# Optimization experiments

Measured on AMD Instinct MI355X. Metric: run time of the kernel, lower is better.

The kernel has to match this reference:

```python
import jax, jax.numpy as jnp
import numpy as np

N = 100000
E = 1600000
IN_CH = 128
HEADS = 4
OUT_CH = 32


def setup_inputs() -> dict:
    key = jax.random.key(0)
    k1, k2, k3, k4, k5, k6 = jax.random.split(key, 6)
    x = jax.random.normal(k1, (N, IN_CH), dtype=jnp.float32)
    edge_attr = jax.random.normal(k2, (E,), dtype=jnp.float32)
    edge_index = jax.random.randint(k3, (2, E), 0, N, dtype=jnp.int64)
    # xavier-uniform-ish parameter init
    def xavier(k, shape):
        fan_in, fan_out = shape[-1], shape[-2] if len(shape) > 1 else shape[-1]
        lim = jnp.sqrt(6.0 / (fan_in + fan_out)).astype(jnp.float32)
        return jax.random.uniform(k, shape, jnp.float32, -lim, lim)
    lin_w = xavier(k4, (HEADS * OUT_CH, IN_CH))       # nn.Linear weight [out,in]
    lin_edge_w = xavier(k5, (HEADS * OUT_CH, 1))      # [out,1]
    att = xavier(k6, (1, HEADS, 3 * OUT_CH))
    return {"x": x, "edge_attr": edge_attr, "edge_index": edge_index,
            "lin_w": lin_w, "lin_edge_w": lin_edge_w, "att": att}


def reference(x, edge_attr, edge_index, lin_w, lin_edge_w, att):
    n = x.shape[0]
    # node transform: [N, H, C]
    xh = (x @ lin_w.T).reshape(n, HEADS, OUT_CH)
    # edge transform: [E, H, C]
    eh = (edge_attr[:, None] @ lin_edge_w.T).reshape(-1, HEADS, OUT_CH)
    row, col = edge_index[0], edge_index[1]
    # split att into source/dest/edge parts to avoid materializing cat([x_i,x_j,e])
    att_i, att_j, att_e = jnp.split(att, 3, axis=-1)  # each [1, H, C]
    # per-edge attention logits: [E, H]
    alpha = ((xh[row] * att_i).sum(-1)
             + (xh[col] * att_j).sum(-1)
             + (eh * att_e).sum(-1))
    alpha = jax.nn.leaky_relu(alpha, negative_slope=0.2)
    # segment softmax over destination node (row)
    amax = jax.ops.segment_max(alpha, row, num_segments=n)           # [N, H]
    amax = jnp.where(jnp.isfinite(amax), amax, 0.0)
    ex = jnp.exp(alpha - amax[row])
    den = jax.ops.segment_sum(ex, row, num_segments=n)               # [N, H]
    alpha = ex / (den[row] + 1e-16)
    # weighted message scatter-add: [N, H, C]
    out = jax.ops.segment_sum(alpha[..., None] * xh[col], row, num_segments=n)
    # concat heads
    return out.reshape(n, HEADS * OUT_CH)
```

## Files before the change

### kernel.cpp

```cpp
#include <hip/hip_runtime.h>

#define HEADS 4
#define OUT_CH 32
#define HC 128
#define INC 128
#define CAP 48

typedef __attribute__((ext_vector_type(8))) short bfrag;
typedef __attribute__((ext_vector_type(4))) float ffrag;

union U16 { uint4 u; bfrag f; };

__device__ __forceinline__ unsigned short f2bf(float f) {
  unsigned int u = __float_as_uint(f);
  unsigned int r = (u + 0x7FFFu + ((u >> 16) & 1u)) >> 16;
  return (unsigned short)r;
}

__global__ __launch_bounds__(256) void prep_kernel(
    const float* __restrict__ W, const float* __restrict__ lew,
    const float* __restrict__ att, unsigned short* __restrict__ Wb,
    float* __restrict__ ce, int* __restrict__ cnt, int N) {
  int bid = blockIdx.x;
  int tid = threadIdx.x;
  if (bid < 16) {
    int i4 = bid * 256 + tid;
    float4 v = ((const float4*)W)[i4];
    ushort4 o;
    o.x = f2bf(v.x);
    o.y = f2bf(v.y);
    o.z = f2bf(v.z);
    o.w = f2bf(v.w);
    ((ushort4*)Wb)[i4] = o;
    if (bid == 0 && tid < HEADS) {
      float s = 0.f;
      for (int c = 0; c < OUT_CH; ++c)
        s += lew[tid * OUT_CH + c] * att[tid * 96 + 2 * OUT_CH + c];
      ce[tid] = s;
    }
  } else {
    int zi = (bid - 16) * 256 + tid;
    int stride = (gridDim.x - 16) * 256;
    for (int i = zi; i < N; i += stride) cnt[i] = 0;
  }
}

#define APITCH 136
__global__ __launch_bounds__(256) void gemm_build(
    const float* __restrict__ x, const unsigned short* __restrict__ Wb,
    const float* __restrict__ att, const int* __restrict__ ei,
    const float* __restrict__ ea, unsigned short* __restrict__ xhb,
    float* __restrict__ si, float* __restrict__ sj, int* __restrict__ cnt,
    unsigned int* __restrict__ slots, int nrows, int E, int G) {
  __shared__ unsigned short Als[4][16 * APITCH];

  if (blockIdx.x >= G) {
    int e = (blockIdx.x - G) * 256 + threadIdx.x;
    if (e < E) {
      int r = ei[e];
      int c = ei[E + e];
      unsigned int u = __float_as_uint(ea[e]);
      unsigned int word = ((u + 0x10000u) & 0xFFFE0000u) | (unsigned int)c;
      int pos = atomicAdd(&cnt[r], 1);
      if (pos < CAP) slots[(size_t)r * CAP + pos] = word;
    }
    return;
  }

  const int tid = threadIdx.x;
  const int wid = tid >> 6;
  const int lane = tid & 63;
  const int row0 = blockIdx.x * 64 + wid * 16;
  if (row0 >= nrows) return;
  unsigned short* As = &Als[wid][0];

#pragma unroll
  for (int t = 0; t < 8; t++) {
    int idx = t * 64 + lane;
    int r = idx >> 5;
    int q = idx & 31;
    int gr = row0 + r;
    float4 v = make_float4(0.f, 0.f, 0.f, 0.f);
    if (gr < nrows) v = ((const float4*)x)[(size_t)gr * 32 + q];
    unsigned int p0 = ((unsigned int)f2bf(v.y) << 16) | f2bf(v.x);
    unsigned int p1 = ((unsigned int)f2bf(v.w) << 16) | f2bf(v.z);
    *(uint2*)&As[r * APITCH + q * 4] = make_uint2(p0, p1);
  }

  const int m15 = lane & 15;
  const int g = lane >> 4;

  ffrag acc[8];
#pragma unroll
  for (int t = 0; t < 8; t++) acc[t] = (ffrag){0.f, 0.f, 0.f, 0.f};

#pragma unroll
  for (int ks = 0; ks < 4; ks++) {
    U16 a;
    a.u = *(const uint4*)&As[m15 * APITCH + ks * 32 + g * 8];
#pragma unroll
    for (int nt = 0; nt < 8; nt++) {
      U16 b;
      b.u = *(const uint4*)&Wb[(size_t)(nt * 16 + m15) * 128 + ks * 32 + g * 8];
      acc[nt] = __builtin_amdgcn_mfma_f32_16x16x32_bf16(a.f, b.f, acc[nt],
                                                        0, 0, 0);
    }
  }

  float ai[8], aj[8];
#pragma unroll
  for (int t = 0; t < 8; t++) {
    int h = t >> 1, c = (t & 1) * 16 + m15;
    ai[t] = att[h * 96 + c];
    aj[t] = att[h * 96 + 32 + c];
  }
#pragma unroll
  for (int reg = 0; reg < 4; reg++) {
    float ph_i[4], ph_j[4];
#pragma unroll
    for (int h = 0; h < 4; h++) {
      ph_i[h] = acc[2 * h][reg] * ai[2 * h] + acc[2 * h + 1][reg] * ai[2 * h + 1];
      ph_j[h] = acc[2 * h][reg] * aj[2 * h] + acc[2 * h + 1][reg] * aj[2 * h + 1];
    }
#pragma unroll
    for (int off = 8; off >= 1; off >>= 1) {
#pragma unroll
      for (int h = 0; h < 4; h++) {
        ph_i[h] += __shfl_down(ph_i[h], off, 16);
        ph_j[h] += __shfl_down(ph_j[h], off, 16);
      }
    }
    int gr = row0 + g * 4 + reg;
    if (m15 == 0 && gr < nrows) {
#pragma unroll
      for (int h = 0; h < 4; h++) {
        si[(size_t)gr * 4 + h] = ph_i[h];
        sj[(size_t)gr * 4 + h] = ph_j[h];
      }
    }
  }

#pragma unroll
  for (int t = 0; t < 8; t++) {
#pragma unroll
    for (int reg = 0; reg < 4; reg++) {
      int r = g * 4 + reg;
      int n = t * 16 + m15;
      As[r * 128 + n] = f2bf(acc[t][reg]);
    }
  }
  const uint4* src = (const uint4*)As;
#pragma unroll
  for (int t = 0; t < 4; t++) {
    int idx = t * 64 + lane;
    int r = idx >> 4, q = idx & 15;
    int gr = row0 + r;
    if (gr < nrows) ((uint4*)(xhb + (size_t)gr * 128))[q] = src[idx];
  }
}

__global__ __launch_bounds__(256) void gather_kernel(
    const int* __restrict__ cnt, const unsigned int* __restrict__ slots,
    const float* __restrict__ si, const float* __restrict__ sj,
    const float* __restrict__ ce, const unsigned short* __restrict__ xhb,
    float* __restrict__ out, int n) {
  __shared__ int cls[4][CAP];
  __shared__ float wls[4][4][CAP];

  int wid = threadIdx.x >> 6;
  int node = blockIdx.x * 4 + wid;
  if (node >= n) return;
  int lane = threadIdx.x & 63;
  int h = lane >> 4;

  int m = cnt[node];
  float4 si4 = *(const float4*)(si + (size_t)node * 4);
  float4 ce4 = *(const float4*)ce;

  if (lane < CAP) {
    unsigned int word = slots[(size_t)node * CAP + lane];
    int c = word & 0x1FFFF;
    if (c >= n) c = 0;
    float eaf = __uint_as_float(word & 0xFFFE0000u);
    float4 sjv = *(const float4*)(sj + (size_t)c * 4);
    float t0 = si4.x + sjv.x + eaf * ce4.x;
    float t1 = si4.y + sjv.y + eaf * ce4.y;
    float t2 = si4.z + sjv.z + eaf * ce4.z;
    float t3 = si4.w + sjv.w + eaf * ce4.w;
    t0 = t0 > 0.f ? t0 : 0.2f * t0;
    t1 = t1 > 0.f ? t1 : 0.2f * t1;
    t2 = t2 > 0.f ? t2 : 0.2f * t2;
    t3 = t3 > 0.f ? t3 : 0.2f * t3;
    bool live = lane < m;
    cls[wid][lane] = live ? c : 0;
    wls[wid][0][lane] = live ? __expf(t0) : 0.f;
    wls[wid][1][lane] = live ? __expf(t1) : 0.f;
    wls[wid][2][lane] = live ? __expf(t2) : 0.f;
    wls[wid][3][lane] = live ? __expf(t3) : 0.f;
  }
  if (m > CAP) m = CAP;
  int mr = (m + 7) & ~7;

  const unsigned short* xb = xhb + lane * 2;
  float acc0 = 0.f, acc1 = 0.f, wsum = 0.f;
  for (int k = 0; k < mr; k += 8) {
    int4 ca = *(const int4*)&cls[wid][k];
    int4 cb = *(const int4*)&cls[wid][k + 4];
    float4 wa = *(const float4*)&wls[wid][h][k];
    float4 wb = *(const float4*)&wls[wid][h][k + 4];
    unsigned int x0 = *(const unsigned int*)(xb + (size_t)ca.x * 128);
    unsigned int x1 = *(const unsigned int*)(xb + (size_t)ca.y * 128);
    unsigned int x2 = *(const unsigned int*)(xb + (size_t)ca.z * 128);
    unsigned int x3 = *(const unsigned int*)(xb + (size_t)ca.w * 128);
    unsigned int x4 = *(const unsigned int*)(xb + (size_t)cb.x * 128);
    unsigned int x5 = *(const unsigned int*)(xb + (size_t)cb.y * 128);
    unsigned int x6 = *(const unsigned int*)(xb + (size_t)cb.z * 128);
    unsigned int x7 = *(const unsigned int*)(xb + (size_t)cb.w * 128);
    acc0 += wa.x * __uint_as_float(x0 << 16) +
            wa.y * __uint_as_float(x1 << 16) +
            wa.z * __uint_as_float(x2 << 16) +
            wa.w * __uint_as_float(x3 << 16) +
            wb.x * __uint_as_float(x4 << 16) +
            wb.y * __uint_as_float(x5 << 16) +
            wb.z * __uint_as_float(x6 << 16) +
            wb.w * __uint_as_float(x7 << 16);
    acc1 += wa.x * __uint_as_float(x0 & 0xFFFF0000u) +
            wa.y * __uint_as_float(x1 & 0xFFFF0000u) +
            wa.z * __uint_as_float(x2 & 0xFFFF0000u) +
            wa.w * __uint_as_float(x3 & 0xFFFF0000u) +
            wb.x * __uint_as_float(x4 & 0xFFFF0000u) +
            wb.y * __uint_as_float(x5 & 0xFFFF0000u) +
            wb.z * __uint_as_float(x6 & 0xFFFF0000u) +
            wb.w * __uint_as_float(x7 & 0xFFFF0000u);
    wsum += wa.x + wa.y + wa.z + wa.w + wb.x + wb.y + wb.z + wb.w;
  }

  float inv = 1.0f / (wsum + 1e-16f);
  float2 o;
  o.x = acc0 * inv;
  o.y = acc1 * inv;
  *(float2*)(out + (size_t)node * HC + lane * 2) = o;
}

extern "C" void kernel_launch(void* const* d_in, const int* in_sizes, int n_in,
                              void* d_out, int out_size, void* d_ws,
                              size_t ws_size, hipStream_t stream) {
  const float* x = (const float*)d_in[0];
  const float* edge_attr = (const float*)d_in[1];
  const int* ei = (const int*)d_in[2];
  const float* lin_w = (const float*)d_in[3];
  const float* lew = (const float*)d_in[4];
  const float* att = (const float*)d_in[5];
  float* out = (float*)d_out;

  const int N = in_sizes[0] / INC;
  const int E = in_sizes[1];

  unsigned int* slots = (unsigned int*)d_ws;
  unsigned short* xhb = (unsigned short*)(slots + (size_t)N * CAP);
  float* si = (float*)(xhb + (size_t)N * 128);
  float* sj = si + (size_t)N * 4;
  float* ce = sj + (size_t)N * 4;
  unsigned short* Wb = (unsigned short*)(ce + 16);
  int* cnt = (int*)(Wb + 16384);

  prep_kernel<<<128, 256, 0, stream>>>(lin_w, lew, att, Wb, ce, cnt, N);

  const int G = (N + 63) / 64;
  const int B = (E + 255) / 256;
  gemm_build<<<G + B, 256, 0, stream>>>(x, Wb, att, ei, edge_attr, xhb, si,
                                        sj, cnt, slots, N, E, G);
  gather_kernel<<<(N + 3) / 4, 256, 0, stream>>>(cnt, slots, si, sj, ce, xhb,
                                                 out, N);
}
```

Baseline: 278.8 us.

## Bucket edges by destination range before atomic slot scatter for locality

Edge binning no longer does random atomics directly. Each wave first partitions its edges into 8 destination-node ranges with ballots and writes them to per-wave queues, reusing the output buffer as scratch. A new scatter kernel then processes one range per block group, so the atomics and slot writes touch a smaller working set that fits better in cache. This adds an extra kernel launch plus queue write/read traffic, and edges past the per-wave capacity fall back to the direct atomic path.

```diff
diff --git a/kernel.cpp b/kernel.cpp
--- a/kernel.cpp
+++ b/kernel.cpp
@@ -5,6 +5,8 @@
 #define HC 128
 #define INC 128
 #define CAP 48
+#define NSL 8
+#define WCAP 28
 
 typedef __attribute__((ext_vector_type(8))) short bfrag;
 typedef __attribute__((ext_vector_type(4))) float ffrag;
@@ -51,18 +53,45 @@
     const float* __restrict__ att, const int* __restrict__ ei,
     const float* __restrict__ ea, unsigned short* __restrict__ xhb,
     float* __restrict__ si, float* __restrict__ sj, int* __restrict__ cnt,
-    unsigned int* __restrict__ slots, int nrows, int E, int G) {
+    unsigned int* __restrict__ slots, unsigned long long* __restrict__ queue,
+    unsigned short* __restrict__ counts, int nrows, int E, int G, int bsz,
+    int NW) {
   __shared__ unsigned short Als[4][16 * APITCH];
 
   if (blockIdx.x >= G) {
-    int e = (blockIdx.x - G) * 256 + threadIdx.x;
-    if (e < E) {
-      int r = ei[e];
+    int bidb = blockIdx.x - G;
+    int e = bidb * 256 + threadIdx.x;
+    int lane = threadIdx.x & 63;
+    int gwave = bidb * 4 + (threadIdx.x >> 6);
+    bool valid = e < E;
+    int r = 0, sl = -1;
+    unsigned int word = 0;
+    unsigned long long rec = 0;
+    if (valid) {
+      r = ei[e];
       int c = ei[E + e];
       unsigned int u = __float_as_uint(ea[e]);
-      unsigned int word = ((u + 0x10000u) & 0xFFFE0000u) | (unsigned int)c;
-      int pos = atomicAdd(&cnt[r], 1);
-      if (pos < CAP) slots[(size_t)r * CAP + pos] = word;
+      word = ((u + 0x10000u) & 0xFFFE0000u) | (unsigned int)c;
+      rec = ((unsigned long long)word << 32) | (unsigned int)r;
+      sl = r / bsz;
+      if (sl > NSL - 1) sl = NSL - 1;
+    }
+#pragma unroll
+    for (int bb = 0; bb < NSL; ++bb) {
+      unsigned long long mask = __ballot(valid && (sl == bb));
+      if (valid && sl == bb) {
+        int rank = __popcll(mask & ((1ull << lane) - 1ull));
+        if (rank < WCAP) {
+          queue[(size_t)(bb * NW + gwave) * WCAP + rank] = rec;
+        } else {
+          int pos = atomicAdd(&cnt[r], 1);
+          if (pos < CAP) slots[(size_t)r * CAP + pos] = word;
+        }
+      }
+      if (lane == 0) {
+        int k = (int)__popcll(mask);
+        counts[bb * NW + gwave] = (unsigned short)(k < WCAP ? k : WCAP);
+      }
     }
     return;
   }
@@ -156,6 +185,27 @@
     int r = idx >> 4, q = idx & 15;
     int gr = row0 + r;
     if (gr < nrows) ((uint4*)(xhb + (size_t)gr * 128))[q] = src[idx];
+  }
+}
+
+__global__ __launch_bounds__(256) void scatter_b(
+    const unsigned long long* __restrict__ queue,
+    const unsigned short* __restrict__ counts, int* __restrict__ cnt,
+    unsigned int* __restrict__ slots, int NW) {
+  int g = blockIdx.x & 7;
+  int blk = blockIdx.x >> 3;
+  int nblk = gridDim.x >> 3;
+  int wid = threadIdx.x >> 6;
+  int lane = threadIdx.x & 63;
+  for (int s = blk * 4 + wid; s < NW; s += nblk * 4) {
+    int k = counts[g * NW + s];
+    if (lane < k) {
+      unsigned long long rec = queue[(size_t)(g * NW + s) * WCAP + lane];
+      int r = (int)(unsigned int)rec;
+      unsigned int word = (unsigned int)(rec >> 32);
+      int pos = atomicAdd(&cnt[r], 1);
+      if (pos < CAP) slots[(size_t)r * CAP + pos] = word;
+    }
   }
 }
 
@@ -264,12 +314,20 @@
   unsigned short* Wb = (unsigned short*)(ce + 16);
   int* cnt = (int*)(Wb + 16384);
 
-  prep_kernel<<<128, 256, 0, stream>>>(lin_w, lew, att, Wb, ce, cnt, N);
-
   const int G = (N + 63) / 64;
   const int B = (E + 255) / 256;
+  const int NW = B * 4;
+  const int bsz = (N + NSL - 1) / NSL;
+
+  unsigned long long* queue = (unsigned long long*)d_out;
+  unsigned short* counts =
+      (unsigned short*)(queue + (size_t)NSL * NW * WCAP);
+
+  prep_kernel<<<128, 256, 0, stream>>>(lin_w, lew, att, Wb, ce, cnt, N);
   gemm_build<<<G + B, 256, 0, stream>>>(x, Wb, att, ei, edge_attr, xhb, si,
-                                        sj, cnt, slots, N, E, G);
+                                        sj, cnt, slots, queue, counts, N, E,
+                                        G, bsz, NW);
+  scatter_b<<<2048, 256, 0, stream>>>(queue, counts, cnt, slots, NW);
   gather_kernel<<<(N + 3) / 4, 256, 0, stream>>>(cnt, slots, si, sj, ce, xhb,
                                                  out, N);
 }
```

Result: slower. 300.7 us (+7.9%).
